# Performance work log

Measured on AMD Instinct MI355X. Metric: run time of the kernel, lower is better.

The kernel has to match this reference:

```python
import jax, jax.numpy as jnp
import numpy as np

N, H, W, C, G, K = 8, 64, 64, 128, 8, 3
GC = C // G          # group channels = 16
P = K * K            # 9 sampling points
PAD = DIL = STRIDE = 1
OS = 1.0             # offset_scale
EPS = 1e-6
H_IN, W_IN = H + 2 * PAD, W + 2 * PAD


def _grid_sample_nhwc(img, grid):
    # img: (B, Hi, Wi, Cc) ; grid: (B, L, Pp, 2) in [-1,1]
    # bilinear, padding_mode='zeros', align_corners=False (matches F.grid_sample)
    B, Hi, Wi, Cc = img.shape
    gx = (grid[..., 0] + 1.0) * (Wi * 0.5) - 0.5
    gy = (grid[..., 1] + 1.0) * (Hi * 0.5) - 0.5
    x0 = jnp.floor(gx)
    y0 = jnp.floor(gy)
    wx1 = gx - x0
    wy1 = gy - y0
    b = jnp.arange(B).reshape(B, 1, 1)

    def tap(xi, yi, wgt):
        valid = (xi >= 0) & (xi <= Wi - 1) & (yi >= 0) & (yi <= Hi - 1)
        xc = jnp.clip(xi, 0, Wi - 1).astype(jnp.int32)
        yc = jnp.clip(yi, 0, Hi - 1).astype(jnp.int32)
        return img[b, yc, xc] * (wgt * valid)[..., None]

    return (tap(x0, y0, (1 - wx1) * (1 - wy1))
            + tap(x0 + 1, y0, wx1 * (1 - wy1))
            + tap(x0, y0 + 1, (1 - wx1) * wy1)
            + tap(x0 + 1, y0 + 1, wx1 * wy1))


def _forward(x, w_in, b_in, dw_w, dw_b, ln_g, ln_b, w_off, b_off, w_msk, b_msk, w_out, b_out):
    n = x.shape[0]
    x_proj = x @ w_in + b_in                                  # input_proj (n,H,W,C)
    # dw_conv: depthwise 3x3 -> LayerNorm(channels_last) -> GELU
    x1 = jax.lax.conv_general_dilated(
        x, dw_w, (1, 1), [((K - 1) // 2,) * 2] * 2,
        dimension_numbers=('NHWC', 'HWIO', 'NHWC'), feature_group_count=C) + dw_b
    mu = jnp.mean(x1, -1, keepdims=True)
    var = jnp.mean((x1 - mu) ** 2, -1, keepdims=True)
    x1 = (x1 - mu) * jax.lax.rsqrt(var + EPS) * ln_g + ln_b
    x1 = jax.nn.gelu(x1, approximate=False)
    offset = x1 @ w_off + b_off                               # (n,H,W,G*P*2)
    mask = jax.nn.softmax((x1 @ w_msk + b_msk).reshape(n, H, W, G, P), axis=-1)
    # reference points on the padded input (pixel-center, normalized)
    ry = (DIL * (K - 1) // 2 + 0.5 + jnp.arange(H, dtype=jnp.float32) * STRIDE) / H_IN
    rx = (DIL * (K - 1) // 2 + 0.5 + jnp.arange(W, dtype=jnp.float32) * STRIDE) / W_IN
    ref = jnp.stack([jnp.broadcast_to(rx[None, :], (H, W)),
                     jnp.broadcast_to(ry[:, None], (H, W))], -1)      # (H,W,2) = (x,y)
    # dilation kernel grid, x-major flatten (matches torch meshgrid indexing='ij')
    ks = jnp.arange(K, dtype=jnp.float32) * DIL - DIL * (K - 1) // 2
    gxk, gyk = jnp.meshgrid(ks, ks, indexing='ij')
    pts = jnp.stack([gxk / W_IN, gyk / H_IN], -1).reshape(P, 2)
    pts = jnp.tile(pts, (G, 1))                                       # (G*P,2), group-major
    loc = (ref[:, :, None, :] + pts[None, None, :, :] * OS).reshape(1, H, W, G * P * 2)
    snorm = jnp.tile(jnp.array([W_IN, H_IN], jnp.float32), G * P)     # [w,h,w,h,...]
    loc = loc + offset * OS / snorm
    grids = (2.0 * loc - 1.0).reshape(n, H * W, G, P, 2)
    grids = grids.transpose(0, 2, 1, 3, 4).reshape(n * G, H * W, P, 2)
    x_pad = jnp.pad(x_proj, ((0, 0), (PAD, PAD), (PAD, PAD), (0, 0)))
    img = x_pad.reshape(n, H_IN, W_IN, G, GC).transpose(0, 3, 1, 2, 4).reshape(n * G, H_IN, W_IN, GC)
    sampled = _grid_sample_nhwc(img, grids)                            # (n*G, HW, P, GC)
    m = mask.reshape(n, H * W, G, P).transpose(0, 2, 1, 3).reshape(n * G, H * W, P)
    out = (sampled * m[..., None]).sum(2)                              # (n*G, HW, GC)
    out = out.reshape(n, G, H * W, GC).transpose(0, 2, 1, 3).reshape(n, H, W, C)
    return out @ w_out + b_out                                         # output_proj


def setup_inputs():
    key = jax.random.key(0)
    k = jax.random.split(key, 8)
    s = 0.02
    f = jnp.float32
    return {
        'x': jax.random.normal(k[0], (N, H, W, C), f),
        'w_in': jax.random.normal(k[1], (C, C), f) * (1.0 / np.sqrt(C)),
        'b_in': jnp.zeros((C,), f),
        'dw_w': jax.random.normal(k[2], (K, K, 1, C), f) * s,
        'dw_b': jnp.zeros((C,), f),
        'ln_g': jnp.ones((C,), f),
        'ln_b': jnp.zeros((C,), f),
        'w_off': jax.random.normal(k[3], (C, G * P * 2), f) * s,
        'b_off': jax.random.normal(k[4], (G * P * 2,), f) * s,
        'w_msk': jax.random.normal(k[5], (C, G * P), f) * s,
        'b_msk': jnp.zeros((G * P,), f),
        'w_out': jax.random.normal(k[6], (C, C), f) * (1.0 / np.sqrt(C)),
        'b_out': jnp.zeros((C,), f),
    }


def reference(x, w_in, b_in, dw_w, dw_b, ln_g, ln_b, w_off, b_off, w_msk, b_msk, w_out, b_out):
    return _forward(x, w_in, b_in, dw_w, dw_b, ln_g, ln_b, w_off, b_off, w_msk, b_msk, w_out, b_out)
```

## Files before the change

kernel.cpp:

```cpp
#include <hip/hip_runtime.h>
#include <math.h>

#define NB 8
#define H 64
#define W 64
#define C 128
#define G 8
#define GC 16
#define P 9
#define NPIX (NB * H * W)
#define N_OFF 144
#define N_MSK 72
#define PXB 32
#define RECW 232
#define PK_IN_ELEMS   (8 * 4 * 64 * 8)
#define PK_COMB_ELEMS (14 * 4 * 64 * 8)
#define PK_OUT_ELEMS  (8 * 4 * 64 * 8)

using bf16x8 = __attribute__((ext_vector_type(8))) short;
using f32x4  = __attribute__((ext_vector_type(4))) float;
using u32x4  = __attribute__((ext_vector_type(4))) unsigned;

__device__ __forceinline__ short f2bf(float f) {
    union { float fv; unsigned u; } v; v.fv = f;
    unsigned r = v.u + 0x7fffu + ((v.u >> 16) & 1u);
    return (short)(r >> 16);
}

__global__ __launch_bounds__(256) void k_pack(
    const float* __restrict__ w_in, const float* __restrict__ w_off,
    const float* __restrict__ w_msk, const float* __restrict__ w_out,
    short* __restrict__ pk_in, short* __restrict__ pk_comb, short* __restrict__ pk_out)
{
    const int tid = blockIdx.x * 256 + threadIdx.x;
    int p, which;
    if (tid < PK_IN_ELEMS) { p = tid; which = 0; }
    else if (tid < PK_IN_ELEMS + PK_COMB_ELEMS) { p = tid - PK_IN_ELEMS; which = 1; }
    else if (tid < PK_IN_ELEMS + PK_COMB_ELEMS + PK_OUT_ELEMS) { p = tid - PK_IN_ELEMS - PK_COMB_ELEMS; which = 2; }
    else return;
    const int e = p & 7, lane = (p >> 3) & 63, kt = (p >> 9) & 3, nt = p >> 11;
    const int k = kt * 32 + (lane >> 4) * 8 + e;
    const int n = nt * 16 + (lane & 15);
    float v;
    if (which == 0) {
        v = w_in[k * C + n];
        pk_in[p] = f2bf(v);
    } else if (which == 1) {
        if (n < N_OFF) v = w_off[k * N_OFF + n];
        else if (n < N_OFF + N_MSK) v = w_msk[k * N_MSK + (n - N_OFF)];
        else v = 0.f;
        pk_comb[p] = f2bf(v);
    } else {
        v = w_out[k * C + n];
        pk_out[p] = f2bf(v);
    }
}

__global__ __launch_bounds__(256, 2) void k_fm(
    const float* __restrict__ x, const float* __restrict__ dw_w,
    const float* __restrict__ dw_b, const float* __restrict__ ln_g,
    const float* __restrict__ ln_b, const short* __restrict__ pk_in,
    const float* __restrict__ b_in, const short* __restrict__ pk_comb,
    const float* __restrict__ b_off, const float* __restrict__ b_msk,
    unsigned short* __restrict__ xproj, float* __restrict__ out)
{
    __shared__ __align__(16) short xa[PXB * C];
    __shared__ __align__(16) short x1s[PXB * C];
    __shared__ unsigned short recs[PXB * RECW];
    __shared__ float part[PXB][8][2];
    __shared__ float stats[PXB][2];

    const int t = threadIdx.x;
    const int n = blockIdx.x & 7;
    const int local = blockIdx.x >> 3;
    const int y = local >> 1;
    const int xb = (local & 1) * PXB;
    const int gpix0 = (n * H + y) * W + xb;

    const int px = t >> 3;
    const int c8 = t & 7;
    const int c0 = c8 * 16;
    const int gpx = gpix0 + px;

    float a[16];
    #pragma unroll
    for (int q = 0; q < 4; ++q) {
        f32x4 v = *(const f32x4*)(dw_b + c0 + q * 4);
        #pragma unroll
        for (int e = 0; e < 4; ++e) a[q * 4 + e] = v[e];
    }
    #pragma unroll
    for (int ky = 0; ky < 3; ++ky) {
        const int yy = y + ky - 1;
        if (yy < 0 || yy >= H) continue;
        #pragma unroll
        for (int kx = 0; kx < 3; ++kx) {
            const int xx = xb + px + kx - 1;
            if (xx < 0 || xx >= W) continue;
            const float* xp = x + ((size_t)(n * H + yy) * W + xx) * C + c0;
            const float* wp = dw_w + (ky * 3 + kx) * C + c0;
            #pragma unroll
            for (int q = 0; q < 4; ++q) {
                f32x4 xv = *(const f32x4*)(xp + q * 4);
                f32x4 wv = *(const f32x4*)(wp + q * 4);
                #pragma unroll
                for (int e = 0; e < 4; ++e)
                    a[q * 4 + e] = fmaf(xv[e], wv[e], a[q * 4 + e]);
            }
        }
    }
    {
        const float* cp = x + (size_t)gpx * C + c0;
        const int sw = (px & 7) << 4;
        #pragma unroll
        for (int h = 0; h < 2; ++h) {
            f32x4 v0 = *(const f32x4*)(cp + h * 8);
            f32x4 v1 = *(const f32x4*)(cp + h * 8 + 4);
            bf16x8 pk;
            #pragma unroll
            for (int e = 0; e < 4; ++e) { pk[e] = f2bf(v0[e]); pk[4 + e] = f2bf(v1[e]); }
            *(bf16x8*)((char*)xa + px * 256 + ((c8 * 32 + h * 16) ^ sw)) = pk;
        }
    }
    {
        float s = 0.f, sq = 0.f;
        #pragma unroll
        for (int cc = 0; cc < 16; ++cc) { s += a[cc]; sq = fmaf(a[cc], a[cc], sq); }
        part[px][c8][0] = s;
        part[px][c8][1] = sq;
    }
    __syncthreads();
    if (t < PXB) {
        float S = 0.f, Q = 0.f;
        #pragma unroll
        for (int q = 0; q < 8; ++q) { S += part[t][q][0]; Q += part[t][q][1]; }
        const float mu = S * (1.f / C);
        const float va = Q * (1.f / C) - mu * mu;
        stats[t][0] = mu;
        stats[t][1] = rsqrtf(va + 1e-6f);
    }
    __syncthreads();
    {
        const float mu = stats[px][0], rs = stats[px][1];
        const int sw = (px & 7) << 4;
        #pragma unroll
        for (int h = 0; h < 2; ++h) {
            bf16x8 pk;
            #pragma unroll
            for (int e = 0; e < 8; ++e) {
                const int cc = h * 8 + e;
                float v = (a[cc] - mu) * rs * ln_g[c0 + cc] + ln_b[c0 + cc];
                pk[e] = f2bf(v * 0.5f * (1.f + erff(v * 0.70710678118654752f)));
            }
            *(bf16x8*)((char*)x1s + px * 256 + ((c8 * 32 + h * 16) ^ sw)) = pk;
        }
    }
    __syncthreads();

    {
        const int w = t >> 6, l = t & 63;
        const int swA = (l & 7) << 4;
        bf16x8 aA[2][4], aB[2][4];
        #pragma unroll
        for (int mt = 0; mt < 2; ++mt) {
            const int m = mt * 16 + (l & 15);
            #pragma unroll
            for (int kt = 0; kt < 4; ++kt) {
                const int byte = m * 256 + ((kt * 64 + (l >> 4) * 16) ^ swA);
                aA[mt][kt] = *(const bf16x8*)((char*)xa + byte);
                aB[mt][kt] = *(const bf16x8*)((char*)x1s + byte);
            }
        }
        #pragma unroll
        for (int i = 0; i < 2; ++i) {
            const int nt = w + i * 4;
            bf16x8 bf[4];
            const short* bp = pk_in + nt * 2048 + l * 8;
            #pragma unroll
            for (int kt = 0; kt < 4; ++kt) bf[kt] = *(const bf16x8*)(bp + kt * 512);
            const float bias = b_in[nt * 16 + (l & 15)];
            #pragma unroll
            for (int mt = 0; mt < 2; ++mt) {
                f32x4 acc = {0.f, 0.f, 0.f, 0.f};
                #pragma unroll
                for (int kt = 0; kt < 4; ++kt)
                    acc = __builtin_amdgcn_mfma_f32_16x16x32_bf16(aA[mt][kt], bf[kt], acc, 0, 0, 0);
                const int prow = gpix0 + mt * 16 + (l >> 4) * 4;
                #pragma unroll
                for (int r = 0; r < 4; ++r)
                    xproj[(size_t)(nt * NPIX + prow + r) * 16 + (l & 15)] =
                        (unsigned short)f2bf(acc[r] + bias);
            }
        }
        #pragma unroll
        for (int i = 0; i < 4; ++i) {
            const int nt = w + i * 4;
            if (nt < 14) {
                bf16x8 bf[4];
                const short* bp = pk_comb + nt * 2048 + l * 8;
                #pragma unroll
                for (int kt = 0; kt < 4; ++kt) bf[kt] = *(const bf16x8*)(bp + kt * 512);
                const int col = nt * 16 + (l & 15);
                int dcol = col;
                float bias = 0.f;
                bool valid = true;
                if (col < N_OFF) bias = b_off[col];
                else {
                    const int cm = col - N_OFF;
                    if (cm < N_MSK) {
                        const int g = (cm * 57) >> 9;
                        dcol = 144 + g * 10 + (cm - 9 * g);
                        bias = b_msk[cm];
                    } else valid = false;
                }
                #pragma unroll
                for (int mt = 0; mt < 2; ++mt) {
                    f32x4 acc = {0.f, 0.f, 0.f, 0.f};
                    #pragma unroll
                    for (int kt = 0; kt < 4; ++kt)
                        acc = __builtin_amdgcn_mfma_f32_16x16x32_bf16(aB[mt][kt], bf[kt], acc, 0, 0, 0);
                    if (valid) {
                        const int pr0 = mt * 16 + (l >> 4) * 4;
                        #pragma unroll
                        for (int r = 0; r < 4; ++r)
                            recs[(pr0 + r) * RECW + dcol] = (unsigned short)f2bf(acc[r] + bias);
                    }
                }
            }
        }
    }
    __syncthreads();

    {
        const int spx = t >> 3, g = t & 7;
        unsigned short* row = recs + spx * RECW + 144 + g * 10;
        float lg[P];
        #pragma unroll
        for (int p = 0; p < P; ++p) lg[p] = __uint_as_float(((unsigned)row[p]) << 16);
        float mx = lg[0];
        #pragma unroll
        for (int p2 = 1; p2 < P; ++p2) mx = fmaxf(mx, lg[p2]);
        float e[P], s = 0.f;
        #pragma unroll
        for (int p2 = 0; p2 < P; ++p2) { e[p2] = expf(lg[p2] - mx); s += e[p2]; }
        const float inv = 1.0f / s;
        #pragma unroll
        for (int p2 = 0; p2 < P; ++p2) row[p2] = (unsigned short)f2bf(e[p2] * inv);
    }
    __syncthreads();

    {
        const int spx = t >> 3, q0 = t & 7;
        const char* srcL = (const char*)recs + spx * (RECW * 2);
        char* dst = (char*)out + (size_t)(gpix0 + spx) * 512;
        #pragma unroll
        for (int h = 0; h < 4; ++h) {
            const int q = q0 + h * 8;
            if (q < 28)
                *(bf16x8*)(dst + q * 16) = *(const bf16x8*)(srcL + q * 16);
        }
    }
}

__global__ __launch_bounds__(256, 2) void k_samp(
    const unsigned short* __restrict__ xproj, const short* __restrict__ pk_out,
    const float* __restrict__ b_out, float* __restrict__ out)
{
    __shared__ __align__(16) short smp[PXB * C];

    const int t = threadIdx.x;
    const int n = blockIdx.x & 7;
    const int local = blockIdx.x >> 3;
    const int y = local >> 1;
    const int xb = (local & 1) * PXB;
    const int gpix0 = (n * H + y) * W + xb;
    const int imgbase = n * (H * W);

    const int spx = t & 31;
    const int g = t >> 5;
    const int xabs = xb + spx;
    const int swz = (spx & 7) << 4;
    const unsigned* slot = (const unsigned*)((const char*)out +
                           (size_t)(gpix0 + spx) * 512);

    float cf[25];
    #pragma unroll
    for (int i = 0; i < 25; ++i) cf[i] = 0.f;
    float amax = 0.f;
    {
        u32x4 a0 = *(const u32x4*)(slot + g * 9);
        u32x4 a1 = *(const u32x4*)(slot + g * 9 + 4);
        const unsigned ov8 = slot[g * 9 + 8];
        u32x4 b0 = *(const u32x4*)(slot + 72 + 5 * g);
        const unsigned pb4 = slot[72 + 5 * g + 4];
        #pragma unroll
        for (int p = 0; p < P; ++p) {
            const unsigned ovp = (p < 4) ? a0[p & 3] : (p < 8) ? a1[p & 3] : ov8;
            const unsigned pu = (p < 8) ? b0[p >> 1] : pb4;
            const float m = (p & 1) ? __uint_as_float(pu & 0xffff0000u)
                                    : __uint_as_float(pu << 16);
            const float ox = __uint_as_float(ovp << 16);
            const float oy = __uint_as_float(ovp & 0xffff0000u);
            amax = fmaxf(amax, fmaxf(fabsf(ox), fabsf(oy)));
            const float fx = floorf(ox);
            const float fy = floorf(oy);
            const float wx = ox - fx, wy = oy - fy;
            const bool lox = fx < -0.5f;
            const bool loy = fy < -0.5f;
            const float wc0 = lox ? (1.f - wx) : 0.f;
            const float wc1 = lox ? wx : (1.f - wx);
            const float wc2 = lox ? 0.f : wx;
            const float wr0 = loy ? (1.f - wy) : 0.f;
            const float wr1 = loy ? wy : (1.f - wy);
            const float wr2 = loy ? 0.f : wy;
            const float mr0 = m * wr0, mr1 = m * wr1, mr2 = m * wr2;
            const int dxp = p / 3 - 1, dyp = p % 3 - 1;
            const int base = (dyp + 1) * 5 + (dxp + 1);
            cf[base + 0]      = fmaf(wc0, mr0, cf[base + 0]);
            cf[base + 1]      = fmaf(wc1, mr0, cf[base + 1]);
            cf[base + 2]      = fmaf(wc2, mr0, cf[base + 2]);
            cf[base + 5]      = fmaf(wc0, mr1, cf[base + 5]);
            cf[base + 6]      = fmaf(wc1, mr1, cf[base + 6]);
            cf[base + 7]      = fmaf(wc2, mr1, cf[base + 7]);
            cf[base + 10]     = fmaf(wc0, mr2, cf[base + 10]);
            cf[base + 11]     = fmaf(wc1, mr2, cf[base + 11]);
            cf[base + 12]     = fmaf(wc2, mr2, cf[base + 12]);
        }
    }
    #pragma unroll
    for (int j = 0; j < 5; ++j) {
        const int xc = xabs + j - 2;
        if (!((xc >= 0) & (xc < W))) {
            #pragma unroll
            for (int i = 0; i < 5; ++i) cf[i * 5 + j] = 0.f;
        }
    }
    #pragma unroll
    for (int i = 0; i < 5; ++i) {
        const int yc = y + i - 2;
        if (!((yc >= 0) & (yc < H))) {
            #pragma unroll
            for (int j = 0; j < 5; ++j) cf[i * 5 + j] = 0.f;
        }
    }

    const char* pb = (const char*)(xproj + (size_t)(g * NPIX + imgbase) * 16);
    int rowoff[5], coloff[5];
    #pragma unroll
    for (int i = 0; i < 5; ++i) {
        rowoff[i] = min(max(y + i - 2, 0), H - 1) * (W * 32);
        coloff[i] = min(max(xabs + i - 2, 0), W - 1) * 32;
    }

    float acc[16];
    #pragma unroll
    for (int q = 0; q < 16; ++q) acc[q] = 0.f;

    if (amax < 1.0f) {
        #pragma unroll
        for (int i = 0; i < 5; ++i) {
            #pragma unroll
            for (int j = 0; j < 5; ++j) {
                const float c = cf[i * 5 + j];
                const char* ap = pb + (rowoff[i] + coloff[j]);
                u32x4 v0 = *(const u32x4*)ap;
                u32x4 v1 = *(const u32x4*)(ap + 16);
                #pragma unroll
                for (int e = 0; e < 4; ++e) {
                    acc[2 * e]     = fmaf(c, __uint_as_float(v0[e] << 16), acc[2 * e]);
                    acc[2 * e + 1] = fmaf(c, __uint_as_float(v0[e] & 0xffff0000u), acc[2 * e + 1]);
                    acc[8 + 2 * e]     = fmaf(c, __uint_as_float(v1[e] << 16), acc[8 + 2 * e]);
                    acc[8 + 2 * e + 1] = fmaf(c, __uint_as_float(v1[e] & 0xffff0000u), acc[8 + 2 * e + 1]);
                }
            }
        }
    } else {
        for (int p = 0; p < P; ++p) {
            const unsigned ovp = slot[g * 9 + p];
            const unsigned pu = slot[72 + 5 * g + (p >> 1)];
            const float m = (p & 1) ? __uint_as_float(pu & 0xffff0000u)
                                    : __uint_as_float(pu << 16);
            const float ux = (float)(xabs + (p / 3) - 1) + __uint_as_float(ovp << 16);
            const float uy = (float)(y + (p % 3) - 1) + __uint_as_float(ovp & 0xffff0000u);
            const float fx = floorf(ux), fy = floorf(uy);
            const float wx = ux - fx, wy = uy - fy;
            const int x0 = (int)fx, y0 = (int)fy;
            float w4[4];
            w4[0] = m * (1.f - wx) * (1.f - wy);
            w4[1] = m * wx * (1.f - wy);
            w4[2] = m * (1.f - wx) * wy;
            w4[3] = m * wx * wy;
            if (!((x0 >= 0) & (x0 < W)))       { w4[0] = 0.f; w4[2] = 0.f; }
            if (!((x0 >= -1) & (x0 < W - 1)))  { w4[1] = 0.f; w4[3] = 0.f; }
            if (!((y0 >= 0) & (y0 < H)))       { w4[0] = 0.f; w4[1] = 0.f; }
            if (!((y0 >= -1) & (y0 < H - 1)))  { w4[2] = 0.f; w4[3] = 0.f; }
            const int xc[2] = { min(max(x0, 0), W - 1), min(max(x0 + 1, 0), W - 1) };
            const int yc[2] = { min(max(y0, 0), H - 1), min(max(y0 + 1, 0), H - 1) };
            for (int cn = 0; cn < 4; ++cn) {
                const float wgt = w4[cn];
                if (wgt == 0.f) continue;
                const char* ap = pb + ((size_t)(yc[cn >> 1] * W + xc[cn & 1]) * 32);
                u32x4 v0 = *(const u32x4*)ap;
                u32x4 v1 = *(const u32x4*)(ap + 16);
                #pragma unroll
                for (int e = 0; e < 4; ++e) {
                    acc[2 * e]     = fmaf(wgt, __uint_as_float(v0[e] << 16), acc[2 * e]);
                    acc[2 * e + 1] = fmaf(wgt, __uint_as_float(v0[e] & 0xffff0000u), acc[2 * e + 1]);
                    acc[8 + 2 * e]     = fmaf(wgt, __uint_as_float(v1[e] << 16), acc[8 + 2 * e]);
                    acc[8 + 2 * e + 1] = fmaf(wgt, __uint_as_float(v1[e] & 0xffff0000u), acc[8 + 2 * e + 1]);
                }
            }
        }
    }

    #pragma unroll
    for (int h = 0; h < 2; ++h) {
        bf16x8 pk;
        #pragma unroll
        for (int e = 0; e < 8; ++e) pk[e] = f2bf(acc[h * 8 + e]);
        *(bf16x8*)((char*)smp + spx * 256 + ((g * 32 + h * 16) ^ swz)) = pk;
    }
    __syncthreads();

    {
        const int w = t >> 6, l = t & 63;
        const int swA = (l & 7) << 4;
        bf16x8 aS[2][4];
        #pragma unroll
        for (int mt = 0; mt < 2; ++mt) {
            const int m = mt * 16 + (l & 15);
            #pragma unroll
            for (int kt = 0; kt < 4; ++kt)
                aS[mt][kt] = *(const bf16x8*)((char*)smp + m * 256 +
                                              ((kt * 64 + (l >> 4) * 16) ^ swA));
        }
        #pragma unroll
        for (int i = 0; i < 2; ++i) {
            const int nt = w + i * 4;
            bf16x8 bf[4];
            const short* bp = pk_out + nt * 2048 + l * 8;
            #pragma unroll
            for (int kt = 0; kt < 4; ++kt) bf[kt] = *(const bf16x8*)(bp + kt * 512);
            const float bias = b_out[nt * 16 + (l & 15)];
            #pragma unroll
            for (int mt = 0; mt < 2; ++mt) {
                f32x4 acc2 = {0.f, 0.f, 0.f, 0.f};
                #pragma unroll
                for (int kt = 0; kt < 4; ++kt)
                    acc2 = __builtin_amdgcn_mfma_f32_16x16x32_bf16(aS[mt][kt], bf[kt], acc2, 0, 0, 0);
                const int row0 = gpix0 + mt * 16 + (l >> 4) * 4;
                #pragma unroll
                for (int r = 0; r < 4; ++r)
                    out[(size_t)(row0 + r) * C + nt * 16 + (l & 15)] = acc2[r] + bias;
            }
        }
    }
}

extern "C" void kernel_launch(void* const* d_in, const int* in_sizes, int n_in,
                              void* d_out, int out_size, void* d_ws, size_t ws_size,
                              hipStream_t stream)
{
    const float* x     = (const float*)d_in[0];
    const float* w_in  = (const float*)d_in[1];
    const float* b_in  = (const float*)d_in[2];
    const float* dw_w  = (const float*)d_in[3];
    const float* dw_b  = (const float*)d_in[4];
    const float* ln_g  = (const float*)d_in[5];
    const float* ln_b  = (const float*)d_in[6];
    const float* w_off = (const float*)d_in[7];
    const float* b_off = (const float*)d_in[8];
    const float* w_msk = (const float*)d_in[9];
    const float* b_msk = (const float*)d_in[10];
    const float* w_out = (const float*)d_in[11];
    const float* b_out = (const float*)d_in[12];

    short* pk_in   = (short*)d_ws;
    short* pk_comb = pk_in + PK_IN_ELEMS;
    short* pk_out  = pk_comb + PK_COMB_ELEMS;
    unsigned short* xproj = (unsigned short*)(pk_out + PK_OUT_ELEMS);
    float* out     = (float*)d_out;

    hipLaunchKernelGGL(k_pack, dim3(240), dim3(256), 0, stream,
                       w_in, w_off, w_msk, w_out, pk_in, pk_comb, pk_out);
    hipLaunchKernelGGL(k_fm, dim3(NPIX / PXB), dim3(256), 0, stream,
                       x, dw_w, dw_b, ln_g, ln_b, pk_in, b_in,
                       pk_comb, b_off, b_msk, xproj, out);
    hipLaunchKernelGGL(k_samp, dim3(NPIX / PXB), dim3(256), 0, stream,
                       xproj, pk_out, b_out, out);
}
```

Baseline: 59.97 us.

## Stage sampling window in shared memory and shuffle-reduce LayerNorm stats

```diff
diff --git a/kernel.cpp b/kernel.cpp
--- a/kernel.cpp
+++ b/kernel.cpp
@@ -67,8 +67,6 @@
     __shared__ __align__(16) short xa[PXB * C];
     __shared__ __align__(16) short x1s[PXB * C];
     __shared__ unsigned short recs[PXB * RECW];
-    __shared__ float part[PXB][8][2];
-    __shared__ float stats[PXB][2];
 
     const int t = threadIdx.x;
     const int n = blockIdx.x & 7;
@@ -79,13 +77,14 @@
 
     const int px = t >> 3;
     const int c8 = t & 7;
-    const int c0 = c8 * 16;
+    const int cb = c8 * 4;
     const int gpx = gpix0 + px;
+    const int sw = (px & 7) << 4;
 
     float a[16];
     #pragma unroll
     for (int q = 0; q < 4; ++q) {
-        f32x4 v = *(const f32x4*)(dw_b + c0 + q * 4);
+        f32x4 v = *(const f32x4*)(dw_b + cb + q * 32);
         #pragma unroll
         for (int e = 0; e < 4; ++e) a[q * 4 + e] = v[e];
     }
@@ -97,12 +96,12 @@
         for (int kx = 0; kx < 3; ++kx) {
             const int xx = xb + px + kx - 1;
             if (xx < 0 || xx >= W) continue;
-            const float* xp = x + ((size_t)(n * H + yy) * W + xx) * C + c0;
-            const float* wp = dw_w + (ky * 3 + kx) * C + c0;
+            const float* xp = x + ((size_t)(n * H + yy) * W + xx) * C;
+            const float* wp = dw_w + (ky * 3 + kx) * C;
             #pragma unroll
             for (int q = 0; q < 4; ++q) {
-                f32x4 xv = *(const f32x4*)(xp + q * 4);
-                f32x4 wv = *(const f32x4*)(wp + q * 4);
+                f32x4 xv = *(const f32x4*)(xp + cb + q * 32);
+                f32x4 wv = *(const f32x4*)(wp + cb + q * 32);
                 #pragma unroll
                 for (int e = 0; e < 4; ++e)
                     a[q * 4 + e] = fmaf(xv[e], wv[e], a[q * 4 + e]);
@@ -110,50 +109,46 @@
         }
     }
     {
-        const float* cp = x + (size_t)gpx * C + c0;
-        const int sw = (px & 7) << 4;
-        #pragma unroll
-        for (int h = 0; h < 2; ++h) {
-            f32x4 v0 = *(const f32x4*)(cp + h * 8);
-            f32x4 v1 = *(const f32x4*)(cp + h * 8 + 4);
-            bf16x8 pk;
-            #pragma unroll
-            for (int e = 0; e < 4; ++e) { pk[e] = f2bf(v0[e]); pk[4 + e] = f2bf(v1[e]); }
-            *(bf16x8*)((char*)xa + px * 256 + ((c8 * 32 + h * 16) ^ sw)) = pk;
-        }
-    }
+        const float* cp = x + (size_t)gpx * C;
+        #pragma unroll
+        for (int q = 0; q < 4; ++q) {
+            f32x4 v = *(const f32x4*)(cp + cb + q * 32);
+            const unsigned lo = ((unsigned)(unsigned short)f2bf(v[0])) |
+                                (((unsigned)(unsigned short)f2bf(v[1])) << 16);
+            const unsigned hi = ((unsigned)(unsigned short)f2bf(v[2])) |
+                                (((unsigned)(unsigned short)f2bf(v[3])) << 16);
+            *(unsigned long long*)((char*)xa + px * 256 + ((cb * 2 + q * 64) ^ sw)) =
+                ((unsigned long long)hi << 32) | lo;
+        }
+    }
+    float mu, rsg;
     {
         float s = 0.f, sq = 0.f;
         #pragma unroll
         for (int cc = 0; cc < 16; ++cc) { s += a[cc]; sq = fmaf(a[cc], a[cc], sq); }
-        part[px][c8][0] = s;
-        part[px][c8][1] = sq;
-    }
-    __syncthreads();
-    if (t < PXB) {
-        float S = 0.f, Q = 0.f;
-        #pragma unroll
-        for (int q = 0; q < 8; ++q) { S += part[t][q][0]; Q += part[t][q][1]; }
-        const float mu = S * (1.f / C);
-        const float va = Q * (1.f / C) - mu * mu;
-        stats[t][0] = mu;
-        stats[t][1] = rsqrtf(va + 1e-6f);
-    }
-    __syncthreads();
-    {
-        const float mu = stats[px][0], rs = stats[px][1];
-        const int sw = (px & 7) << 4;
-        #pragma unroll
-        for (int h = 0; h < 2; ++h) {
-            bf16x8 pk;
-            #pragma unroll
-            for (int e = 0; e < 8; ++e) {
-                const int cc = h * 8 + e;
-                float v = (a[cc] - mu) * rs * ln_g[c0 + cc] + ln_b[c0 + cc];
-                pk[e] = f2bf(v * 0.5f * (1.f + erff(v * 0.70710678118654752f)));
-            }
-            *(bf16x8*)((char*)x1s + px * 256 + ((c8 * 32 + h * 16) ^ sw)) = pk;
-        }
+        #pragma unroll
+        for (int d = 1; d < 8; d <<= 1) {
+            s += __shfl_xor(s, d);
+            sq += __shfl_xor(sq, d);
+        }
+        mu = s * (1.f / C);
+        const float va = sq * (1.f / C) - mu * mu;
+        rsg = rsqrtf(va + 1e-6f);
+    }
+    #pragma unroll
+    for (int q = 0; q < 4; ++q) {
+        f32x4 gv = *(const f32x4*)(ln_g + cb + q * 32);
+        f32x4 bv = *(const f32x4*)(ln_b + cb + q * 32);
+        unsigned short h4[4];
+        #pragma unroll
+        for (int e = 0; e < 4; ++e) {
+            float v = (a[q * 4 + e] - mu) * rsg * gv[e] + bv[e];
+            h4[e] = (unsigned short)f2bf(v * 0.5f * (1.f + erff(v * 0.70710678118654752f)));
+        }
+        const unsigned lo = ((unsigned)h4[0]) | (((unsigned)h4[1]) << 16);
+        const unsigned hi = ((unsigned)h4[2]) | (((unsigned)h4[3]) << 16);
+        *(unsigned long long*)((char*)x1s + px * 256 + ((cb * 2 + q * 64) ^ sw)) =
+            ((unsigned long long)hi << 32) | lo;
     }
     __syncthreads();
 
@@ -262,11 +257,13 @@
     }
 }
 
+#define PADX 41
 __global__ __launch_bounds__(256, 2) void k_samp(
     const unsigned short* __restrict__ xproj, const short* __restrict__ pk_out,
     const float* __restrict__ b_out, float* __restrict__ out)
 {
     __shared__ __align__(16) short smp[PXB * C];
+    __shared__ __align__(16) u32x4 win[2 * 4 * 5 * PADX];
 
     const int t = threadIdx.x;
     const int n = blockIdx.x & 7;
@@ -277,148 +274,152 @@
     const int imgbase = n * (H * W);
 
     const int spx = t & 31;
-    const int g = t >> 5;
+    const int gl = (t >> 5) & 3;
+    const int half = t >> 7;
     const int xabs = xb + spx;
     const int swz = (spx & 7) << 4;
     const unsigned* slot = (const unsigned*)((const char*)out +
                            (size_t)(gpix0 + spx) * 512);
 
-    float cf[25];
-    #pragma unroll
-    for (int i = 0; i < 25; ++i) cf[i] = 0.f;
-    float amax = 0.f;
-    {
-        u32x4 a0 = *(const u32x4*)(slot + g * 9);
-        u32x4 a1 = *(const u32x4*)(slot + g * 9 + 4);
-        const unsigned ov8 = slot[g * 9 + 8];
-        u32x4 b0 = *(const u32x4*)(slot + 72 + 5 * g);
-        const unsigned pb4 = slot[72 + 5 * g + 4];
-        #pragma unroll
-        for (int p = 0; p < P; ++p) {
-            const unsigned ovp = (p < 4) ? a0[p & 3] : (p < 8) ? a1[p & 3] : ov8;
-            const unsigned pu = (p < 8) ? b0[p >> 1] : pb4;
-            const float m = (p & 1) ? __uint_as_float(pu & 0xffff0000u)
-                                    : __uint_as_float(pu << 16);
-            const float ox = __uint_as_float(ovp << 16);
-            const float oy = __uint_as_float(ovp & 0xffff0000u);
-            amax = fmaxf(amax, fmaxf(fabsf(ox), fabsf(oy)));
-            const float fx = floorf(ox);
-            const float fy = floorf(oy);
-            const float wx = ox - fx, wy = oy - fy;
-            const bool lox = fx < -0.5f;
-            const bool loy = fy < -0.5f;
-            const float wc0 = lox ? (1.f - wx) : 0.f;
-            const float wc1 = lox ? wx : (1.f - wx);
-            const float wc2 = lox ? 0.f : wx;
-            const float wr0 = loy ? (1.f - wy) : 0.f;
-            const float wr1 = loy ? wy : (1.f - wy);
-            const float wr2 = loy ? 0.f : wy;
-            const float mr0 = m * wr0, mr1 = m * wr1, mr2 = m * wr2;
-            const int dxp = p / 3 - 1, dyp = p % 3 - 1;
-            const int base = (dyp + 1) * 5 + (dxp + 1);
-            cf[base + 0]      = fmaf(wc0, mr0, cf[base + 0]);
-            cf[base + 1]      = fmaf(wc1, mr0, cf[base + 1]);
-            cf[base + 2]      = fmaf(wc2, mr0, cf[base + 2]);
-            cf[base + 5]      = fmaf(wc0, mr1, cf[base + 5]);
-            cf[base + 6]      = fmaf(wc1, mr1, cf[base + 6]);
-            cf[base + 7]      = fmaf(wc2, mr1, cf[base + 7]);
-            cf[base + 10]     = fmaf(wc0, mr2, cf[base + 10]);
-            cf[base + 11]     = fmaf(wc1, mr2, cf[base + 11]);
-            cf[base + 12]     = fmaf(wc2, mr2, cf[base + 12]);
-        }
-    }
-    #pragma unroll
-    for (int j = 0; j < 5; ++j) {
-        const int xc = xabs + j - 2;
-        if (!((xc >= 0) & (xc < W))) {
-            #pragma unroll
-            for (int i = 0; i < 5; ++i) cf[i * 5 + j] = 0.f;
-        }
-    }
-    #pragma unroll
-    for (int i = 0; i < 5; ++i) {
-        const int yc = y + i - 2;
-        if (!((yc >= 0) & (yc < H))) {
-            #pragma unroll
-            for (int j = 0; j < 5; ++j) cf[i * 5 + j] = 0.f;
-        }
-    }
-
-    const char* pb = (const char*)(xproj + (size_t)(g * NPIX + imgbase) * 16);
-    int rowoff[5], coloff[5];
-    #pragma unroll
-    for (int i = 0; i < 5; ++i) {
-        rowoff[i] = min(max(y + i - 2, 0), H - 1) * (W * 32);
-        coloff[i] = min(max(xabs + i - 2, 0), W - 1) * 32;
-    }
-
-    float acc[16];
-    #pragma unroll
-    for (int q = 0; q < 16; ++q) acc[q] = 0.f;
-
-    if (amax < 1.0f) {
+    for (int f = 0; f < 2; ++f) {
+        const int g = f * 4 + gl;
+
+        float cf[25];
+        #pragma unroll
+        for (int i = 0; i < 25; ++i) cf[i] = 0.f;
+        float amax = 0.f;
+        {
+            u32x4 a0 = *(const u32x4*)(slot + g * 9);
+            u32x4 a1 = *(const u32x4*)(slot + g * 9 + 4);
+            const unsigned ov8 = slot[g * 9 + 8];
+            u32x4 b0 = *(const u32x4*)(slot + 72 + 5 * g);
+            const unsigned pb4 = slot[72 + 5 * g + 4];
+            #pragma unroll
+            for (int p = 0; p < P; ++p) {
+                const unsigned ovp = (p < 4) ? a0[p & 3] : (p < 8) ? a1[p & 3] : ov8;
+                const unsigned pu = (p < 8) ? b0[p >> 1] : pb4;
+                const float m = (p & 1) ? __uint_as_float(pu & 0xffff0000u)
+                                        : __uint_as_float(pu << 16);
+                const float ox = __uint_as_float(ovp << 16);
+                const float oy = __uint_as_float(ovp & 0xffff0000u);
+                amax = fmaxf(amax, fmaxf(fabsf(ox), fabsf(oy)));
+                const float fx = floorf(ox);
+                const float fy = floorf(oy);
+                const float wx = ox - fx, wy = oy - fy;
+                const bool lox = fx < -0.5f;
+                const bool loy = fy < -0.5f;
+                const float wc0 = lox ? (1.f - wx) : 0.f;
+                const float wc1 = lox ? wx : (1.f - wx);
+                const float wc2 = lox ? 0.f : wx;
+                const float wr0 = loy ? (1.f - wy) : 0.f;
+                const float wr1 = loy ? wy : (1.f - wy);
+                const float wr2 = loy ? 0.f : wy;
+                const float mr0 = m * wr0, mr1 = m * wr1, mr2 = m * wr2;
+                const int dxp = p / 3 - 1, dyp = p % 3 - 1;
+                const int base = (dyp + 1) * 5 + (dxp + 1);
+                cf[base + 0]  = fmaf(wc0, mr0, cf[base + 0]);
+                cf[base + 1]  = fmaf(wc1, mr0, cf[base + 1]);
+                cf[base + 2]  = fmaf(wc2, mr0, cf[base + 2]);
+                cf[base + 5]  = fmaf(wc0, mr1, cf[base + 5]);
+                cf[base + 6]  = fmaf(wc1, mr1, cf[base + 6]);
+                cf[base + 7]  = fmaf(wc2, mr1, cf[base + 7]);
+                cf[base + 10] = fmaf(wc0, mr2, cf[base + 10]);
+                cf[base + 11] = fmaf(wc1, mr2, cf[base + 11]);
+                cf[base + 12] = fmaf(wc2, mr2, cf[base + 12]);
+            }
+        }
+        #pragma unroll
+        for (int j = 0; j < 5; ++j) {
+            const int xc = xabs + j - 2;
+            if (!((xc >= 0) & (xc < W))) {
+                #pragma unroll
+                for (int i = 0; i < 5; ++i) cf[i * 5 + j] = 0.f;
+            }
+        }
         #pragma unroll
         for (int i = 0; i < 5; ++i) {
-            #pragma unroll
-            for (int j = 0; j < 5; ++j) {
-                const float c = cf[i * 5 + j];
-                const char* ap = pb + (rowoff[i] + coloff[j]);
-                u32x4 v0 = *(const u32x4*)ap;
-                u32x4 v1 = *(const u32x4*)(ap + 16);
-                #pragma unroll
-                for (int e = 0; e < 4; ++e) {
-                    acc[2 * e]     = fmaf(c, __uint_as_float(v0[e] << 16), acc[2 * e]);
-                    acc[2 * e + 1] = fmaf(c, __uint_as_float(v0[e] & 0xffff0000u), acc[2 * e + 1]);
-                    acc[8 + 2 * e]     = fmaf(c, __uint_as_float(v1[e] << 16), acc[8 + 2 * e]);
-                    acc[8 + 2 * e + 1] = fmaf(c, __uint_as_float(v1[e] & 0xffff0000u), acc[8 + 2 * e + 1]);
+            const int yc = y + i - 2;
+            if (!((yc >= 0) & (yc < H))) {
+                #pragma unroll
+                for (int j = 0; j < 5; ++j) cf[i * 5 + j] = 0.f;
+            }
+        }
+        __syncthreads();
+
+        for (int e = t; e < 1600; e += 256) {
+            const int uh = e & 1;
+            const int v = e >> 1;
+            const int xs = v % 40;
+            const int q2 = v / 40;
+            const int rs = q2 % 5;
+            const int gs = q2 / 5;
+            const int row = min(max(y - 2 + rs, 0), H - 1);
+            const int col = min(max(xb - 4 + xs, 0), W - 1);
+            win[((uh * 4 + gs) * 5 + rs) * PADX + xs] =
+                *(const u32x4*)(xproj +
+                    ((size_t)((f * 4 + gs) * NPIX + imgbase + row * W + col)) * 16 + uh * 8);
+        }
+        __syncthreads();
+
+        {
+            float acc[8];
+            #pragma unroll
+            for (int q = 0; q < 8; ++q) acc[q] = 0.f;
+            if (amax < 1.0f) {
+                const u32x4* wb = win + (half * 4 + gl) * 5 * PADX + spx + 2;
+                #pragma unroll
+                for (int rr = 0; rr < 5; ++rr) {
+                    #pragma unroll
+                    for (int cc = 0; cc < 5; ++cc) {
+                        const float c = cf[rr * 5 + cc];
+                        const u32x4 v = wb[rr * PADX + cc];
+                        #pragma unroll
+                        for (int e = 0; e < 4; ++e) {
+                            acc[2 * e]     = fmaf(c, __uint_as_float(v[e] << 16), acc[2 * e]);
+                            acc[2 * e + 1] = fmaf(c, __uint_as_float(v[e] & 0xffff0000u), acc[2 * e + 1]);
+                        }
+                    }
                 }
-            }
-        }
-    } else {
-        for (int p = 0; p < P; ++p) {
-            const unsigned ovp = slot[g * 9 + p];
-            const unsigned pu = slot[72 + 5 * g + (p >> 1)];
-            const float m = (p & 1) ? __uint_as_float(pu & 0xffff0000u)
-                                    : __uint_as_float(pu << 16);
-            const float ux = (float)(xabs + (p / 3) - 1) + __uint_as_float(ovp << 16);
-            const float uy = (float)(y + (p % 3) - 1) + __uint_as_float(ovp & 0xffff0000u);
-            const float fx = floorf(ux), fy = floorf(uy);
-            const float wx = ux - fx, wy = uy - fy;
-            const int x0 = (int)fx, y0 = (int)fy;
-            float w4[4];
-            w4[0] = m * (1.f - wx) * (1.f - wy);
-            w4[1] = m * wx * (1.f - wy);
-            w4[2] = m * (1.f - wx) * wy;
-            w4[3] = m * wx * wy;
-            if (!((x0 >= 0) & (x0 < W)))       { w4[0] = 0.f; w4[2] = 0.f; }
-            if (!((x0 >= -1) & (x0 < W - 1)))  { w4[1] = 0.f; w4[3] = 0.f; }
-            if (!((y0 >= 0) & (y0 < H)))       { w4[0] = 0.f; w4[1] = 0.f; }
-            if (!((y0 >= -1) & (y0 < H - 1)))  { w4[2] = 0.f; w4[3] = 0.f; }
-            const int xc[2] = { min(max(x0, 0), W - 1), min(max(x0 + 1, 0), W - 1) };
-            const int yc[2] = { min(max(y0, 0), H - 1), min(max(y0 + 1, 0), H - 1) };
-            for (int cn = 0; cn < 4; ++cn) {
-                const float wgt = w4[cn];
-                if (wgt == 0.f) continue;
-                const char* ap = pb + ((size_t)(yc[cn >> 1] * W + xc[cn & 1]) * 32);
-                u32x4 v0 = *(const u32x4*)ap;
-                u32x4 v1 = *(const u32x4*)(ap + 16);
-                #pragma unroll
-                for (int e = 0; e < 4; ++e) {
-                    acc[2 * e]     = fmaf(wgt, __uint_as_float(v0[e] << 16), acc[2 * e]);
-                    acc[2 * e + 1] = fmaf(wgt, __uint_as_float(v0[e] & 0xffff0000u), acc[2 * e + 1]);
-                    acc[8 + 2 * e]     = fmaf(wgt, __uint_as_float(v1[e] << 16), acc[8 + 2 * e]);
-                    acc[8 + 2 * e + 1] = fmaf(wgt, __uint_as_float(v1[e] & 0xffff0000u), acc[8 + 2 * e + 1]);
+            } else {
+                const u32x4* plane4 = (const u32x4*)(xproj + (size_t)(g * NPIX + imgbase) * 16);
+                for (int p = 0; p < P; ++p) {
+                    const unsigned ovp = slot[g * 9 + p];
+                    const unsigned pu = slot[72 + 5 * g + (p >> 1)];
+                    const float m = (p & 1) ? __uint_as_float(pu & 0xffff0000u)
+                                            : __uint_as_float(pu << 16);
+                    const float ux = (float)(xabs + (p / 3) - 1) + __uint_as_float(ovp << 16);
+                    const float uy = (float)(y + (p % 3) - 1) + __uint_as_float(ovp & 0xffff0000u);
+                    const float fx = floorf(ux), fy = floorf(uy);
+                    const float wx = ux - fx, wy = uy - fy;
+                    const int x0 = (int)fx, y0 = (int)fy;
+                    float w4[4];
+                    w4[0] = m * (1.f - wx) * (1.f - wy);
+                    w4[1] = m * wx * (1.f - wy);
+                    w4[2] = m * (1.f - wx) * wy;
+                    w4[3] = m * wx * wy;
+                    if (!((x0 >= 0) & (x0 < W)))       { w4[0] = 0.f; w4[2] = 0.f; }
+                    if (!((x0 >= -1) & (x0 < W - 1)))  { w4[1] = 0.f; w4[3] = 0.f; }
+                    if (!((y0 >= 0) & (y0 < H)))       { w4[0] = 0.f; w4[1] = 0.f; }
+                    if (!((y0 >= -1) & (y0 < H - 1)))  { w4[2] = 0.f; w4[3] = 0.f; }
+                    const int xc[2] = { min(max(x0, 0), W - 1), min(max(x0 + 1, 0), W - 1) };
+                    const int yc[2] = { min(max(y0, 0), H - 1), min(max(y0 + 1, 0), H - 1) };
+                    for (int cn = 0; cn < 4; ++cn) {
+                        const float wgt = w4[cn];
+                        if (wgt == 0.f) continue;
+                        const u32x4 v = plane4[(size_t)(yc[cn >> 1] * W + xc[cn & 1]) * 2 + half];
+                        #pragma unroll
+                        for (int e = 0; e < 4; ++e) {
+                            acc[2 * e]     = fmaf(wgt, __uint_as_float(v[e] << 16), acc[2 * e]);
+                            acc[2 * e + 1] = fmaf(wgt, __uint_as_float(v[e] & 0xffff0000u), acc[2 * e + 1]);
+                        }
+                    }
                 }
             }
-        }
-    }
-
-    #pragma unroll
-    for (int h = 0; h < 2; ++h) {
-        bf16x8 pk;
-        #pragma unroll
-        for (int e = 0; e < 8; ++e) pk[e] = f2bf(acc[h * 8 + e]);
-        *(bf16x8*)((char*)smp + spx * 256 + ((g * 32 + h * 16) ^ swz)) = pk;
+            bf16x8 pk;
+            #pragma unroll
+            for (int e = 0; e < 8; ++e) pk[e] = f2bf(acc[e]);
+            *(bf16x8*)((char*)smp + spx * 256 + ((g * 32 + half * 16) ^ swz)) = pk;
+        }
     }
     __syncthreads();
 
```

Result: faster. 50.46 us (-15.9%).
